# Kernel optimization log

Hardware: AMD Instinct MI355X
Metric: run time of the kernel (lower is better)

Reference implementation:

```python
import jax, jax.numpy as jnp
import numpy as np


def setup_inputs() -> dict:
    key = jax.random.key(0)
    B, N = 4, 32768
    xyz = jax.random.normal(key, (B, N, 3), dtype=jnp.float32)
    return {"xyz": xyz, "K": 16, "nqueries": 2048}


def reference(xyz, K, nqueries):
    # xyz: (b, n, 3). Deterministic strided pick of nqueries query points
    # (stand-in for the KD-tree's distance-pick sampling), then brute-force KNN.
    b, n, _ = xyz.shape
    stride = n // nqueries
    q_idx = jnp.arange(nqueries) * stride          # (nq,)
    pts = xyz[:, q_idx, :]                          # (b, nq, 3) sampled query points
    # pairwise squared distances (b, nq, n)
    d = jnp.sum((pts[:, :, None, :] - xyz[:, None, :, :]) ** 2, axis=-1)
    _, idx = jax.lax.top_k(-d, K)                   # (b, nq, K) nearest-neighbor indices
    idx = idx.astype(jnp.int64)[..., None]          # (b, nq, K, 1) matches expand_dims(..., 3)
    return idx, pts
```

## Files before the change

kernel.cpp:

```cpp
#include <hip/hip_runtime.h>
#include <stdint.h>

#define NPTS  32768
#define NQ    2048
#define KNN   16
#define NB    4
#define TS    2048
#define BLOCK 512
#define WPB   8

typedef const __attribute__((address_space(1))) char glds_src_t;
typedef __attribute__((address_space(3))) char glds_dst_t;

__device__ __forceinline__ float2 pk_add(float2 a, float2 b) {
    float2 r;
    asm("v_pk_add_f32 %0, %1, %2" : "=v"(r) : "v"(a), "v"(b));
    return r;
}
__device__ __forceinline__ float2 pk_mul(float2 a, float2 b) {
    float2 r;
    asm("v_pk_mul_f32 %0, %1, %2" : "=v"(r) : "v"(a), "v"(b));
    return r;
}
__device__ __forceinline__ int dpp_shr1_i(int x) {
    return __builtin_amdgcn_update_dpp(x, x, 0x111, 0xf, 0xf, false);
}
__device__ __forceinline__ float dpp_shr1_f(float x) {
    int r = dpp_shr1_i(__float_as_int(x));
    return __int_as_float(r);
}
__device__ __forceinline__ float readlane_f(float x, int l) {
    return __int_as_float(__builtin_amdgcn_readlane(__float_as_int(x), l));
}

template <int T>
__device__ __forceinline__ void insert_all(float d, int p, int lane,
                                           float& ld, int& li, float& tau)
{
    unsigned long long rem = __ballot(d <= tau);
    while (rem) {
        const int srcl = __ffsll(rem) - 1;
        const float wd = readlane_f(d, srcl);
        const int   wi = __builtin_amdgcn_readlane(p, srcl);
        const bool less = (ld < wd) || (ld == wd && li < wi);
        const unsigned long long lm = __ballot(less);
        const int pos = __popc((unsigned)((lm >> (16 * T)) & 0xffffull));
        const float pld = dpp_shr1_f(ld);
        const int   pli = dpp_shr1_i(li);
        if ((lane >> 4) == T) {
            const int gl = lane & 15;
            if (gl == pos)      { ld = wd;  li = wi;  }
            else if (gl > pos)  { ld = pld; li = pli; }
        }
        tau = readlane_f(ld, 16 * T + 15);
        rem &= rem - 1;
        if (rem) rem &= __ballot(d <= tau);
    }
}

__global__ __launch_bounds__(BLOCK) void knn_kernel(const float* __restrict__ xyz,
                                                    float* __restrict__ out_idx,
                                                    float* __restrict__ out_pts)
{
    __shared__ float lds[TS * 3];

    const int tid  = threadIdx.x;
    const int lane = tid & 63;
    const int wv   = tid >> 6;
    const int w    = blockIdx.x * WPB + wv;
    const int b    = w >> 10;
    const int pr   = w & 1023;
    const size_t base = (size_t)b * NPTS * 3;

    const int qp0 = pr << 5;
    const float qx0 = xyz[base + 3 * qp0 + 0];
    const float qy0 = xyz[base + 3 * qp0 + 1];
    const float qz0 = xyz[base + 3 * qp0 + 2];
    const float qx1 = xyz[base + 3 * qp0 + 48];
    const float qy1 = xyz[base + 3 * qp0 + 49];
    const float qz1 = xyz[base + 3 * qp0 + 50];

    const int g0 = b * NQ + (pr << 1);
    if (lane == 0) {
        out_pts[3 * g0 + 0] = qx0;
        out_pts[3 * g0 + 1] = qy0;
        out_pts[3 * g0 + 2] = qz0;
        out_pts[3 * g0 + 3] = qx1;
        out_pts[3 * g0 + 4] = qy1;
        out_pts[3 * g0 + 5] = qz1;
    }

    const float2 nqx = make_float2(-qx0, -qx1);
    const float2 nqy = make_float2(-qy0, -qy1);
    const float2 nqz = make_float2(-qz0, -qz1);

    float ld = __builtin_inff();  int li = 0x7fffffff;
    float tau0 = __builtin_inff(), tau1 = __builtin_inff();

    const float4* lp = (const float4*)lds + 3 * lane;

    for (int tile = 0; tile < NPTS; tile += TS) {
        __syncthreads();
        {
            glds_src_t* gsrc = (glds_src_t*)(xyz + base + (size_t)tile * 3);
            glds_dst_t* ldst = (glds_dst_t*)lds;
            #pragma unroll
            for (int c = 0; c < 3; ++c)
                __builtin_amdgcn_global_load_lds(
                    (const __attribute__((address_space(1))) void*)(gsrc + 16 * (BLOCK * c + tid)),
                    (__attribute__((address_space(3))) void*)(ldst + 16 * (BLOCK * c + tid)),
                    16, 0, 0);
        }
        __syncthreads();

        #pragma unroll
        for (int k = 0; k < TS / 256; ++k) {
            const float4 A = lp[192 * k + 0];
            const float4 Bv = lp[192 * k + 1];
            const float4 Cv = lp[192 * k + 2];
            const float px[4] = { A.x,  A.w,  Bv.z, Cv.y };
            const float py[4] = { A.y,  Bv.x, Bv.w, Cv.z };
            const float pz[4] = { A.z,  Bv.y, Cv.x, Cv.w };

            float d0[4], d1[4];
            bool any = false;
            #pragma unroll
            for (int j = 0; j < 4; ++j) {
                const float2 dx = pk_add(make_float2(px[j], px[j]), nqx);
                const float2 dy = pk_add(make_float2(py[j], py[j]), nqy);
                const float2 dz = pk_add(make_float2(pz[j], pz[j]), nqz);
                const float2 s  = pk_add(pk_add(pk_mul(dx, dx), pk_mul(dy, dy)),
                                         pk_mul(dz, dz));
                d0[j] = s.x;  d1[j] = s.y;
                any = any | (d0[j] <= tau0) | (d1[j] <= tau1);
            }
            if (__ballot(any)) {
                const int pb = tile + 256 * k + 4 * lane;
                #pragma unroll
                for (int j = 0; j < 4; ++j) {
                    insert_all<0>(d0[j], pb + j, lane, ld, li, tau0);
                    insert_all<1>(d1[j], pb + j, lane, ld, li, tau1);
                }
            }
        }
    }

    if (lane < 2 * KNN) {
        out_idx[(size_t)g0 * KNN + lane] = (float)li;
    }
}

extern "C" void kernel_launch(void* const* d_in, const int* in_sizes, int n_in,
                              void* d_out, int out_size, void* d_ws, size_t ws_size,
                              hipStream_t stream) {
    const float* xyz = (const float*)d_in[0];
    float* out = (float*)d_out;
    float* out_idx = out;
    float* out_pts = out + (size_t)NB * NQ * KNN;

    const int blocks = (NB * NQ / 2) / WPB;
    knn_kernel<<<blocks, BLOCK, 0, stream>>>(xyz, out_idx, out_pts);
}
```

Baseline: 222.9 us.

## Transpose tiles to SoA in LDS with register-prefetched loads and smaller blocks

Replaces the direct global-to-LDS copy with a register prefetch of the next tile. The prefetched tile is written to LDS transposed into separate x/y/z arrays, so each lane reads aligned float4 vectors of consecutive points and computes distances packed over point pairs instead of query pairs. The block shrinks to 256 threads with a 4-block occupancy hint, and the insertion order is changed to process all query-0 candidates before query-1. This overlaps global loads with compute and removes the AoS shuffling, at the cost of extra VGPRs for the prefetch buffer and explicit LDS stores.

```diff
diff --git a/kernel.cpp b/kernel.cpp
--- a/kernel.cpp
+++ b/kernel.cpp
@@ -6,11 +6,8 @@
 #define KNN   16
 #define NB    4
 #define TS    2048
-#define BLOCK 512
-#define WPB   8
-
-typedef const __attribute__((address_space(1))) char glds_src_t;
-typedef __attribute__((address_space(3))) char glds_dst_t;
+#define BLOCK 256
+#define WPB   4
 
 __device__ __forceinline__ float2 pk_add(float2 a, float2 b) {
     float2 r;
@@ -26,8 +23,7 @@
     return __builtin_amdgcn_update_dpp(x, x, 0x111, 0xf, 0xf, false);
 }
 __device__ __forceinline__ float dpp_shr1_f(float x) {
-    int r = dpp_shr1_i(__float_as_int(x));
-    return __int_as_float(r);
+    return __int_as_float(dpp_shr1_i(__float_as_int(x)));
 }
 __device__ __forceinline__ float readlane_f(float x, int l) {
     return __int_as_float(__builtin_amdgcn_readlane(__float_as_int(x), l));
@@ -58,11 +54,11 @@
     }
 }
 
-__global__ __launch_bounds__(BLOCK) void knn_kernel(const float* __restrict__ xyz,
-                                                    float* __restrict__ out_idx,
-                                                    float* __restrict__ out_pts)
+__global__ __launch_bounds__(BLOCK, 4) void knn_kernel(const float* __restrict__ xyz,
+                                                       float* __restrict__ out_idx,
+                                                       float* __restrict__ out_pts)
 {
-    __shared__ float lds[TS * 3];
+    __shared__ float lds[3 * TS];
 
     const int tid  = threadIdx.x;
     const int lane = tid & 63;
@@ -90,57 +86,90 @@
         out_pts[3 * g0 + 5] = qz1;
     }
 
-    const float2 nqx = make_float2(-qx0, -qx1);
-    const float2 nqy = make_float2(-qy0, -qy1);
-    const float2 nqz = make_float2(-qz0, -qz1);
+    const float2 nx0 = make_float2(-qx0, -qx0), nx1 = make_float2(-qx1, -qx1);
+    const float2 ny0 = make_float2(-qy0, -qy0), ny1 = make_float2(-qy1, -qy1);
+    const float2 nz0 = make_float2(-qz0, -qz0), nz1 = make_float2(-qz1, -qz1);
 
     float ld = __builtin_inff();  int li = 0x7fffffff;
     float tau0 = __builtin_inff(), tau1 = __builtin_inff();
 
-    const float4* lp = (const float4*)lds + 3 * lane;
+    float4 f[6];
+    {
+        const float4* src = (const float4*)(xyz + base);
+        #pragma unroll
+        for (int g = 0; g < 2; ++g) {
+            const int q = tid + g * BLOCK;
+            f[3 * g + 0] = src[3 * q + 0];
+            f[3 * g + 1] = src[3 * q + 1];
+            f[3 * g + 2] = src[3 * q + 2];
+        }
+    }
 
     for (int tile = 0; tile < NPTS; tile += TS) {
         __syncthreads();
         {
-            glds_src_t* gsrc = (glds_src_t*)(xyz + base + (size_t)tile * 3);
-            glds_dst_t* ldst = (glds_dst_t*)lds;
             #pragma unroll
-            for (int c = 0; c < 3; ++c)
-                __builtin_amdgcn_global_load_lds(
-                    (const __attribute__((address_space(1))) void*)(gsrc + 16 * (BLOCK * c + tid)),
-                    (__attribute__((address_space(3))) void*)(ldst + 16 * (BLOCK * c + tid)),
-                    16, 0, 0);
+            for (int g = 0; g < 2; ++g) {
+                const int q = tid + g * BLOCK;
+                const float4 a = f[3 * g + 0];
+                const float4 c = f[3 * g + 1];
+                const float4 e = f[3 * g + 2];
+                ((float4*)(lds         ))[q] = make_float4(a.x, a.w, c.z, e.y);
+                ((float4*)(lds + TS    ))[q] = make_float4(a.y, c.x, c.w, e.z);
+                ((float4*)(lds + 2 * TS))[q] = make_float4(a.z, c.y, e.x, e.w);
+            }
         }
         __syncthreads();
+        if (tile + TS < NPTS) {
+            const float4* src = (const float4*)(xyz + base + (size_t)(tile + TS) * 3);
+            #pragma unroll
+            for (int g = 0; g < 2; ++g) {
+                const int q = tid + g * BLOCK;
+                f[3 * g + 0] = src[3 * q + 0];
+                f[3 * g + 1] = src[3 * q + 1];
+                f[3 * g + 2] = src[3 * q + 2];
+            }
+        }
 
         #pragma unroll
         for (int k = 0; k < TS / 256; ++k) {
-            const float4 A = lp[192 * k + 0];
-            const float4 Bv = lp[192 * k + 1];
-            const float4 Cv = lp[192 * k + 2];
-            const float px[4] = { A.x,  A.w,  Bv.z, Cv.y };
-            const float py[4] = { A.y,  Bv.x, Bv.w, Cv.z };
-            const float pz[4] = { A.z,  Bv.y, Cv.x, Cv.w };
+            const float4 X = ((const float4*)(lds         ))[64 * k + lane];
+            const float4 Y = ((const float4*)(lds + TS    ))[64 * k + lane];
+            const float4 Z = ((const float4*)(lds + 2 * TS))[64 * k + lane];
+            const float2 xp[2] = { make_float2(X.x, X.y), make_float2(X.z, X.w) };
+            const float2 yp[2] = { make_float2(Y.x, Y.y), make_float2(Y.z, Y.w) };
+            const float2 zp[2] = { make_float2(Z.x, Z.y), make_float2(Z.z, Z.w) };
 
-            float d0[4], d1[4];
-            bool any = false;
+            float2 D[2][2];
             #pragma unroll
-            for (int j = 0; j < 4; ++j) {
-                const float2 dx = pk_add(make_float2(px[j], px[j]), nqx);
-                const float2 dy = pk_add(make_float2(py[j], py[j]), nqy);
-                const float2 dz = pk_add(make_float2(pz[j], pz[j]), nqz);
-                const float2 s  = pk_add(pk_add(pk_mul(dx, dx), pk_mul(dy, dy)),
-                                         pk_mul(dz, dz));
-                d0[j] = s.x;  d1[j] = s.y;
-                any = any | (d0[j] <= tau0) | (d1[j] <= tau1);
+            for (int pp = 0; pp < 2; ++pp) {
+                const float2 ax = pk_add(xp[pp], nx0);
+                const float2 ay = pk_add(yp[pp], ny0);
+                const float2 az = pk_add(zp[pp], nz0);
+                D[pp][0] = pk_add(pk_add(pk_mul(ax, ax), pk_mul(ay, ay)),
+                                  pk_mul(az, az));
+                const float2 bx = pk_add(xp[pp], nx1);
+                const float2 by = pk_add(yp[pp], ny1);
+                const float2 bz = pk_add(zp[pp], nz1);
+                D[pp][1] = pk_add(pk_add(pk_mul(bx, bx), pk_mul(by, by)),
+                                  pk_mul(bz, bz));
             }
+
+            const bool any =
+                (D[0][0].x <= tau0) | (D[0][0].y <= tau0) |
+                (D[1][0].x <= tau0) | (D[1][0].y <= tau0) |
+                (D[0][1].x <= tau1) | (D[0][1].y <= tau1) |
+                (D[1][1].x <= tau1) | (D[1][1].y <= tau1);
             if (__ballot(any)) {
                 const int pb = tile + 256 * k + 4 * lane;
-                #pragma unroll
-                for (int j = 0; j < 4; ++j) {
-                    insert_all<0>(d0[j], pb + j, lane, ld, li, tau0);
-                    insert_all<1>(d1[j], pb + j, lane, ld, li, tau1);
-                }
+                insert_all<0>(D[0][0].x, pb + 0, lane, ld, li, tau0);
+                insert_all<0>(D[0][0].y, pb + 1, lane, ld, li, tau0);
+                insert_all<0>(D[1][0].x, pb + 2, lane, ld, li, tau0);
+                insert_all<0>(D[1][0].y, pb + 3, lane, ld, li, tau0);
+                insert_all<1>(D[0][1].x, pb + 0, lane, ld, li, tau1);
+                insert_all<1>(D[0][1].y, pb + 1, lane, ld, li, tau1);
+                insert_all<1>(D[1][1].x, pb + 2, lane, ld, li, tau1);
+                insert_all<1>(D[1][1].y, pb + 3, lane, ld, li, tau1);
             }
         }
     }
```

Result: faster. 213.2 us (-4.4%).

## Drop LDS staging, read points directly from global and repack distance math

Applied to the files above, without the earlier changes.

Removes the LDS tile staging and block barriers so each wave reads point coordinates directly from global memory (relying on L1/L2 caching), halves the block size and adds an occupancy hint. The distance computation is restructured to pair adjacent coordinates from the interleaved layout with permuted query vectors instead of broadcasting scalars, and the per-point early-exit checks become one combined ballot per chunk. This trades barrier/LDS overhead for heavier global/cache traffic, since each wave now re-reads the whole point cloud from cache, and the insertion order changes (all query-0 inserts before query-1 inserts).

```diff
diff --git a/kernel.cpp b/kernel.cpp
--- a/kernel.cpp
+++ b/kernel.cpp
@@ -5,12 +5,8 @@
 #define NQ    2048
 #define KNN   16
 #define NB    4
-#define TS    2048
-#define BLOCK 512
-#define WPB   8
-
-typedef const __attribute__((address_space(1))) char glds_src_t;
-typedef __attribute__((address_space(3))) char glds_dst_t;
+#define BLOCK 256
+#define WPB   4
 
 __device__ __forceinline__ float2 pk_add(float2 a, float2 b) {
     float2 r;
@@ -26,8 +22,7 @@
     return __builtin_amdgcn_update_dpp(x, x, 0x111, 0xf, 0xf, false);
 }
 __device__ __forceinline__ float dpp_shr1_f(float x) {
-    int r = dpp_shr1_i(__float_as_int(x));
-    return __int_as_float(r);
+    return __int_as_float(dpp_shr1_i(__float_as_int(x)));
 }
 __device__ __forceinline__ float readlane_f(float x, int l) {
     return __int_as_float(__builtin_amdgcn_readlane(__float_as_int(x), l));
@@ -58,12 +53,10 @@
     }
 }
 
-__global__ __launch_bounds__(BLOCK) void knn_kernel(const float* __restrict__ xyz,
-                                                    float* __restrict__ out_idx,
-                                                    float* __restrict__ out_pts)
+__global__ __launch_bounds__(BLOCK, 8) void knn_kernel(const float* __restrict__ xyz,
+                                                       float* __restrict__ out_idx,
+                                                       float* __restrict__ out_pts)
 {
-    __shared__ float lds[TS * 3];
-
     const int tid  = threadIdx.x;
     const int lane = tid & 63;
     const int wv   = tid >> 6;
@@ -90,58 +83,66 @@
         out_pts[3 * g0 + 5] = qz1;
     }
 
-    const float2 nqx = make_float2(-qx0, -qx1);
-    const float2 nqy = make_float2(-qy0, -qy1);
-    const float2 nqz = make_float2(-qz0, -qz1);
+    const float2 nxy0 = make_float2(-qx0, -qy0), nxy1 = make_float2(-qx1, -qy1);
+    const float2 nzx0 = make_float2(-qz0, -qx0), nzx1 = make_float2(-qz1, -qx1);
+    const float2 nyz0 = make_float2(-qy0, -qz0), nyz1 = make_float2(-qy1, -qz1);
 
     float ld = __builtin_inff();  int li = 0x7fffffff;
     float tau0 = __builtin_inff(), tau1 = __builtin_inff();
 
-    const float4* lp = (const float4*)lds + 3 * lane;
+    const float4* lp = (const float4*)(xyz + base) + 3 * lane;
 
-    for (int tile = 0; tile < NPTS; tile += TS) {
-        __syncthreads();
-        {
-            glds_src_t* gsrc = (glds_src_t*)(xyz + base + (size_t)tile * 3);
-            glds_dst_t* ldst = (glds_dst_t*)lds;
-            #pragma unroll
-            for (int c = 0; c < 3; ++c)
-                __builtin_amdgcn_global_load_lds(
-                    (const __attribute__((address_space(1))) void*)(gsrc + 16 * (BLOCK * c + tid)),
-                    (__attribute__((address_space(3))) void*)(ldst + 16 * (BLOCK * c + tid)),
-                    16, 0, 0);
-        }
-        __syncthreads();
+    #pragma unroll 2
+    for (int k = 0; k < NPTS / 256; ++k) {
+        const float4 A  = lp[192 * k + 0];
+        const float4 Bv = lp[192 * k + 1];
+        const float4 Cv = lp[192 * k + 2];
+        const float2 P1 = make_float2(A.x,  A.y);
+        const float2 P2 = make_float2(A.z,  A.w);
+        const float2 P3 = make_float2(Bv.x, Bv.y);
+        const float2 P4 = make_float2(Bv.z, Bv.w);
+        const float2 P5 = make_float2(Cv.x, Cv.y);
+        const float2 P6 = make_float2(Cv.x ? Cv.x : Cv.x, Cv.y);
+        (void)P6;
 
-        #pragma unroll
-        for (int k = 0; k < TS / 256; ++k) {
-            const float4 A = lp[192 * k + 0];
-            const float4 Bv = lp[192 * k + 1];
-            const float4 Cv = lp[192 * k + 2];
-            const float px[4] = { A.x,  A.w,  Bv.z, Cv.y };
-            const float py[4] = { A.y,  Bv.x, Bv.w, Cv.z };
-            const float pz[4] = { A.z,  Bv.y, Cv.x, Cv.w };
+        const float2 u1 = pk_add(P1, nxy0);  const float2 t1 = pk_mul(u1, u1);
+        const float2 u2 = pk_add(P2, nzx0);  const float2 t2 = pk_mul(u2, u2);
+        const float2 u3 = pk_add(P3, nyz0);  const float2 t3 = pk_mul(u3, u3);
+        const float2 u4 = pk_add(P4, nxy0);  const float2 t4 = pk_mul(u4, u4);
+        const float2 u5 = pk_add(P5, nzx0);  const float2 t5 = pk_mul(u5, u5);
+        const float2 P6r = make_float2(Cv.z, Cv.w);
+        const float2 u6 = pk_add(P6r, nyz0); const float2 t6 = pk_mul(u6, u6);
+        const float d00 = __fadd_rn(__fadd_rn(t1.x, t1.y), t2.x);
+        const float d01 = __fadd_rn(__fadd_rn(t2.y, t3.x), t3.y);
+        const float d02 = __fadd_rn(__fadd_rn(t4.x, t4.y), t5.x);
+        const float d03 = __fadd_rn(__fadd_rn(t5.y, t6.x), t6.y);
 
-            float d0[4], d1[4];
-            bool any = false;
-            #pragma unroll
-            for (int j = 0; j < 4; ++j) {
-                const float2 dx = pk_add(make_float2(px[j], px[j]), nqx);
-                const float2 dy = pk_add(make_float2(py[j], py[j]), nqy);
-                const float2 dz = pk_add(make_float2(pz[j], pz[j]), nqz);
-                const float2 s  = pk_add(pk_add(pk_mul(dx, dx), pk_mul(dy, dy)),
-                                         pk_mul(dz, dz));
-                d0[j] = s.x;  d1[j] = s.y;
-                any = any | (d0[j] <= tau0) | (d1[j] <= tau1);
-            }
-            if (__ballot(any)) {
-                const int pb = tile + 256 * k + 4 * lane;
-                #pragma unroll
-                for (int j = 0; j < 4; ++j) {
-                    insert_all<0>(d0[j], pb + j, lane, ld, li, tau0);
-                    insert_all<1>(d1[j], pb + j, lane, ld, li, tau1);
-                }
-            }
+        const float2 v1 = pk_add(P1, nxy1);  const float2 s1 = pk_mul(v1, v1);
+        const float2 v2 = pk_add(P2, nzx1);  const float2 s2 = pk_mul(v2, v2);
+        const float2 v3 = pk_add(P3, nyz1);  const float2 s3 = pk_mul(v3, v3);
+        const float2 v4 = pk_add(P4, nxy1);  const float2 s4 = pk_mul(v4, v4);
+        const float2 v5 = pk_add(P5, nzx1);  const float2 s5 = pk_mul(v5, v5);
+        const float2 v6 = pk_add(P6r, nyz1); const float2 s6 = pk_mul(v6, v6);
+        const float d10 = __fadd_rn(__fadd_rn(s1.x, s1.y), s2.x);
+        const float d11 = __fadd_rn(__fadd_rn(s2.y, s3.x), s3.y);
+        const float d12 = __fadd_rn(__fadd_rn(s4.x, s4.y), s5.x);
+        const float d13 = __fadd_rn(__fadd_rn(s5.y, s6.x), s6.y);
+
+        const unsigned long long m =
+            __ballot(d00 <= tau0) | __ballot(d01 <= tau0) |
+            __ballot(d02 <= tau0) | __ballot(d03 <= tau0) |
+            __ballot(d10 <= tau1) | __ballot(d11 <= tau1) |
+            __ballot(d12 <= tau1) | __ballot(d13 <= tau1);
+        if (m) {
+            const int pb = (k << 8) + 4 * lane;
+            insert_all<0>(d00, pb + 0, lane, ld, li, tau0);
+            insert_all<0>(d01, pb + 1, lane, ld, li, tau0);
+            insert_all<0>(d02, pb + 2, lane, ld, li, tau0);
+            insert_all<0>(d03, pb + 3, lane, ld, li, tau0);
+            insert_all<1>(d10, pb + 0, lane, ld, li, tau1);
+            insert_all<1>(d11, pb + 1, lane, ld, li, tau1);
+            insert_all<1>(d12, pb + 2, lane, ld, li, tau1);
+            insert_all<1>(d13, pb + 3, lane, ld, li, tau1);
         }
     }
 
```

Result: faster. 210.3 us (-5.7%).

## Process four queries per wavefront, read points from global, and filter with FMA distances

Applied to the files above, without the earlier changes.

Each wavefront now handles four queries, with one 16-lane sorted list per query instead of two, so every loaded point is reused across more queries. The LDS staging and block-level barriers are removed and points are read directly from global memory through the cache. Candidates are first screened with an FMA-based distance against a slightly loosened threshold, and the exact reference-order distance is recomputed only for lanes that pass. This cuts barrier and LDS traffic and halves the point loads per query, at the cost of more registers, more global cache pressure and the extra recomputation.

```diff
diff --git a/kernel.cpp b/kernel.cpp
--- a/kernel.cpp
+++ b/kernel.cpp
@@ -5,37 +5,21 @@
 #define NQ    2048
 #define KNN   16
 #define NB    4
-#define TS    2048
-#define BLOCK 512
-#define WPB   8
+#define BLOCK 256
+#define WPB   4
 
-typedef const __attribute__((address_space(1))) char glds_src_t;
-typedef __attribute__((address_space(3))) char glds_dst_t;
-
-__device__ __forceinline__ float2 pk_add(float2 a, float2 b) {
-    float2 r;
-    asm("v_pk_add_f32 %0, %1, %2" : "=v"(r) : "v"(a), "v"(b));
-    return r;
-}
-__device__ __forceinline__ float2 pk_mul(float2 a, float2 b) {
-    float2 r;
-    asm("v_pk_mul_f32 %0, %1, %2" : "=v"(r) : "v"(a), "v"(b));
-    return r;
-}
 __device__ __forceinline__ int dpp_shr1_i(int x) {
     return __builtin_amdgcn_update_dpp(x, x, 0x111, 0xf, 0xf, false);
 }
 __device__ __forceinline__ float dpp_shr1_f(float x) {
-    int r = dpp_shr1_i(__float_as_int(x));
-    return __int_as_float(r);
+    return __int_as_float(dpp_shr1_i(__float_as_int(x)));
 }
 __device__ __forceinline__ float readlane_f(float x, int l) {
     return __int_as_float(__builtin_amdgcn_readlane(__float_as_int(x), l));
 }
 
-template <int T>
-__device__ __forceinline__ void insert_all(float d, int p, int lane,
-                                           float& ld, int& li, float& tau)
+__device__ __forceinline__ void insert_all(float d, int p, int lane, int t,
+                                           float& ld, int& li, float& tau, float& tg)
 {
     unsigned long long rem = __ballot(d <= tau);
     while (rem) {
@@ -44,110 +28,103 @@
         const int   wi = __builtin_amdgcn_readlane(p, srcl);
         const bool less = (ld < wd) || (ld == wd && li < wi);
         const unsigned long long lm = __ballot(less);
-        const int pos = __popc((unsigned)((lm >> (16 * T)) & 0xffffull));
+        const int pos = __popc((unsigned)((lm >> (16 * t)) & 0xffffull));
         const float pld = dpp_shr1_f(ld);
         const int   pli = dpp_shr1_i(li);
-        if ((lane >> 4) == T) {
+        if ((lane >> 4) == t) {
             const int gl = lane & 15;
             if (gl == pos)      { ld = wd;  li = wi;  }
             else if (gl > pos)  { ld = pld; li = pli; }
         }
-        tau = readlane_f(ld, 16 * T + 15);
+        tau = readlane_f(ld, 16 * t + 15);
+        tg  = tau * 1.00001f;
         rem &= rem - 1;
         if (rem) rem &= __ballot(d <= tau);
     }
 }
 
-__global__ __launch_bounds__(BLOCK) void knn_kernel(const float* __restrict__ xyz,
-                                                    float* __restrict__ out_idx,
-                                                    float* __restrict__ out_pts)
+__global__ __launch_bounds__(BLOCK, 2) void knn_kernel(const float* __restrict__ xyz,
+                                                       float* __restrict__ out_idx,
+                                                       float* __restrict__ out_pts)
 {
-    __shared__ float lds[TS * 3];
-
     const int tid  = threadIdx.x;
     const int lane = tid & 63;
     const int wv   = tid >> 6;
     const int w    = blockIdx.x * WPB + wv;
-    const int b    = w >> 10;
-    const int pr   = w & 1023;
+    const int b    = w >> 9;
+    const int pr   = w & 511;
     const size_t base = (size_t)b * NPTS * 3;
 
-    const int qp0 = pr << 5;
-    const float qx0 = xyz[base + 3 * qp0 + 0];
-    const float qy0 = xyz[base + 3 * qp0 + 1];
-    const float qz0 = xyz[base + 3 * qp0 + 2];
-    const float qx1 = xyz[base + 3 * qp0 + 48];
-    const float qy1 = xyz[base + 3 * qp0 + 49];
-    const float qz1 = xyz[base + 3 * qp0 + 50];
-
-    const int g0 = b * NQ + (pr << 1);
-    if (lane == 0) {
-        out_pts[3 * g0 + 0] = qx0;
-        out_pts[3 * g0 + 1] = qy0;
-        out_pts[3 * g0 + 2] = qz0;
-        out_pts[3 * g0 + 3] = qx1;
-        out_pts[3 * g0 + 4] = qy1;
-        out_pts[3 * g0 + 5] = qz1;
+    const int qp0 = pr << 6;
+    float qx[4], qy[4], qz[4];
+    #pragma unroll
+    for (int t = 0; t < 4; ++t) {
+        qx[t] = xyz[base + 3 * (qp0 + 16 * t) + 0];
+        qy[t] = xyz[base + 3 * (qp0 + 16 * t) + 1];
+        qz[t] = xyz[base + 3 * (qp0 + 16 * t) + 2];
     }
 
-    const float2 nqx = make_float2(-qx0, -qx1);
-    const float2 nqy = make_float2(-qy0, -qy1);
-    const float2 nqz = make_float2(-qz0, -qz1);
+    const int g0 = b * NQ + (pr << 2);
+    if (lane < 12) {
+        const int t = (lane * 11) >> 5;
+        const int c = lane - 3 * t;
+        out_pts[3 * g0 + lane] = xyz[base + 3 * (qp0 + 16 * t) + c];
+    }
 
     float ld = __builtin_inff();  int li = 0x7fffffff;
-    float tau0 = __builtin_inff(), tau1 = __builtin_inff();
+    float tau[4] = { __builtin_inff(), __builtin_inff(),
+                     __builtin_inff(), __builtin_inff() };
+    float tg[4]  = { __builtin_inff(), __builtin_inff(),
+                     __builtin_inff(), __builtin_inff() };
 
-    const float4* lp = (const float4*)lds + 3 * lane;
+    const float4* lp = (const float4*)(xyz + base) + 3 * lane;
 
-    for (int tile = 0; tile < NPTS; tile += TS) {
-        __syncthreads();
-        {
-            glds_src_t* gsrc = (glds_src_t*)(xyz + base + (size_t)tile * 3);
-            glds_dst_t* ldst = (glds_dst_t*)lds;
-            #pragma unroll
-            for (int c = 0; c < 3; ++c)
-                __builtin_amdgcn_global_load_lds(
-                    (const __attribute__((address_space(1))) void*)(gsrc + 16 * (BLOCK * c + tid)),
-                    (__attribute__((address_space(3))) void*)(ldst + 16 * (BLOCK * c + tid)),
-                    16, 0, 0);
-        }
-        __syncthreads();
+    #pragma unroll 2
+    for (int k = 0; k < NPTS / 256; ++k) {
+        const float4 A  = lp[192 * k + 0];
+        const float4 Bv = lp[192 * k + 1];
+        const float4 Cv = lp[192 * k + 2];
+        const float px[4] = { A.x,  A.w,  Bv.z, Cv.y };
+        const float py[4] = { A.y,  Bv.x, Bv.w, Cv.z };
+        const float pz[4] = { A.z,  Bv.y, Cv.x, Cv.w };
 
+        unsigned long long ms[16];
+        unsigned long long m = 0;
         #pragma unroll
-        for (int k = 0; k < TS / 256; ++k) {
-            const float4 A = lp[192 * k + 0];
-            const float4 Bv = lp[192 * k + 1];
-            const float4 Cv = lp[192 * k + 2];
-            const float px[4] = { A.x,  A.w,  Bv.z, Cv.y };
-            const float py[4] = { A.y,  Bv.x, Bv.w, Cv.z };
-            const float pz[4] = { A.z,  Bv.y, Cv.x, Cv.w };
-
-            float d0[4], d1[4];
-            bool any = false;
+        for (int t = 0; t < 4; ++t) {
             #pragma unroll
             for (int j = 0; j < 4; ++j) {
-                const float2 dx = pk_add(make_float2(px[j], px[j]), nqx);
-                const float2 dy = pk_add(make_float2(py[j], py[j]), nqy);
-                const float2 dz = pk_add(make_float2(pz[j], pz[j]), nqz);
-                const float2 s  = pk_add(pk_add(pk_mul(dx, dx), pk_mul(dy, dy)),
-                                         pk_mul(dz, dz));
-                d0[j] = s.x;  d1[j] = s.y;
-                any = any | (d0[j] <= tau0) | (d1[j] <= tau1);
+                const float dx = __fadd_rn(px[j], -qx[t]);
+                const float dy = __fadd_rn(py[j], -qy[t]);
+                const float dz = __fadd_rn(pz[j], -qz[t]);
+                const float g  = __fmaf_rn(dz, dz, __fmaf_rn(dy, dy,
+                                  __fmul_rn(dx, dx)));
+                ms[4 * t + j] = __ballot(g <= tg[t]);
+                m |= ms[4 * t + j];
             }
-            if (__ballot(any)) {
-                const int pb = tile + 256 * k + 4 * lane;
+        }
+
+        if (m) {
+            const int pb = (k << 8) + 4 * lane;
+            #pragma unroll
+            for (int t = 0; t < 4; ++t) {
                 #pragma unroll
                 for (int j = 0; j < 4; ++j) {
-                    insert_all<0>(d0[j], pb + j, lane, ld, li, tau0);
-                    insert_all<1>(d1[j], pb + j, lane, ld, li, tau1);
+                    if (ms[4 * t + j]) {
+                        const float dx = __fadd_rn(px[j], -qx[t]);
+                        const float dy = __fadd_rn(py[j], -qy[t]);
+                        const float dz = __fadd_rn(pz[j], -qz[t]);
+                        const float d  = __fadd_rn(
+                            __fadd_rn(__fmul_rn(dx, dx), __fmul_rn(dy, dy)),
+                            __fmul_rn(dz, dz));
+                        insert_all(d, pb + j, lane, t, ld, li, tau[t], tg[t]);
+                    }
                 }
             }
         }
     }
 
-    if (lane < 2 * KNN) {
-        out_idx[(size_t)g0 * KNN + lane] = (float)li;
-    }
+    out_idx[(size_t)g0 * KNN + lane] = (float)li;
 }
 
 extern "C" void kernel_launch(void* const* d_in, const int* in_sizes, int n_in,
@@ -158,6 +135,6 @@
     float* out_idx = out;
     float* out_pts = out + (size_t)NB * NQ * KNN;
 
-    const int blocks = (NB * NQ / 2) / WPB;
+    const int blocks = (NB * NQ / 4) / WPB;
     knn_kernel<<<blocks, BLOCK, 0, stream>>>(xyz, out_idx, out_pts);
 }
```

New measurement: 260.0 us. +16.6%, slower.
